# Optimization experiments

Hardware: AMD Instinct MI355X
Metric: run time of the kernel (lower is better)

## Reference

```python
import jax, jax.numpy as jnp
import numpy as np

LEVELS = 3


def _wavelet_pyramid(x, levels=LEVELS):
    """Faithful jax port of WaveletTransform.forward.

    Per level: take top-left (H/2^l, W/2^l) region, convolve with the 3x3
    separable low-pass kernel outer([.25,.5,.25]) using zero-padded 'same'
    conv (kernel is symmetric so scipy's flip is a no-op), then write the
    2x-strided downsample into the top-left quarter.
    """
    B, C, H, W = x.shape
    k1 = jnp.array([0.25, 0.5, 0.25], dtype=x.dtype)
    K = jnp.outer(k1, k1)[None, None]  # [1,1,3,3] low_pass.T @ low_pass
    result = x
    for level in range(levels):
        sh, sw = H // (2 ** level), W // (2 ** level)
        if min(sh, sw) <= 2:
            break
        # fold B,C into batch: per-channel 2D conv, zero boundary = scipy 'same'
        temp = result[:, :, :sh, :sw].reshape(B * C, 1, sh, sw)
        approx = jax.lax.conv_general_dilated(
            temp, K, window_strides=(1, 1), padding='SAME',
            dimension_numbers=('NCHW', 'OIHW', 'NCHW'))
        down = approx[:, :, ::2, ::2][:, :, :sh // 2, :sw // 2]
        result = result.at[:, :, :sh // 2, :sw // 2].set(
            down.reshape(B, C, sh // 2, sw // 2))
    return result


def setup_inputs() -> dict:
    key = jax.random.key(0)
    x = jax.random.normal(key, (8, 32, 512, 512), dtype=jnp.float32)
    return {"x": x}


def reference(x):
    return _wavelet_pyramid(x, LEVELS)
```

## Files before the change

### kernel.cpp

```cpp
#include <hip/hip_runtime.h>

#define W 512
#define IMG (512 * 512)
#define NIMG 256

__global__ __launch_bounds__(256) void kA(const float* __restrict__ x,
                                          float* __restrict__ out) {
    const int gid = blockIdx.x;
    const int img = gid >> 8;
    const int b   = gid & 255;
    const int tid = threadIdx.x;
    const int i = (b >> 2) * 4 + (tid >> 6);
    const int j = (b & 3) * 64 + (tid & 63);

    const float* xi = x + (size_t)img * IMG;
    float* oi = out + (size_t)img * IMG;

    const int r0 = 2 * i - 1, r1 = 2 * i, r2 = 2 * i + 1;
    const int c0 = 2 * j - 1;

    float2 m1 = *(const float2*)(xi + r1 * W + 2 * j);
    float2 m2 = *(const float2*)(xi + r2 * W + 2 * j);
    float2 m0 = (r0 >= 0) ? *(const float2*)(xi + r0 * W + 2 * j)
                          : make_float2(0.f, 0.f);
    float l0 = (r0 >= 0 && c0 >= 0) ? xi[r0 * W + c0] : 0.f;
    float l1 = (c0 >= 0) ? xi[r1 * W + c0] : 0.f;
    float l2 = (c0 >= 0) ? xi[r2 * W + c0] : 0.f;

    float h0 = 0.25f * l0 + 0.5f * m0.x + 0.25f * m0.y;
    float h1 = 0.25f * l1 + 0.5f * m1.x + 0.25f * m1.y;
    float h2 = 0.25f * l2 + 0.5f * m2.x + 0.25f * m2.y;
    oi[i * W + j] = 0.25f * h0 + 0.5f * h1 + 0.25f * h2;

    if (i >= 128 || j >= 128) {
        *(float2*)(oi + r1 * W + 2 * j) = m1;
        *(float2*)(oi + r2 * W + 2 * j) = m2;
    }
}

__global__ __launch_bounds__(1024) void kBC(float* __restrict__ out) {
    __shared__ float S1[128][128];
    const int img = blockIdx.x;
    float* oi = out + (size_t)img * IMG;
    const int tid = threadIdx.x;
    const int j = tid & 127;
    const int i0 = tid >> 7;

    for (int k = 0; k < 16; ++k) {
        const int i = i0 + 8 * k;
        const int r0 = 2 * i - 1, r1 = 2 * i, r2 = 2 * i + 1;
        const int c0 = 2 * j - 1;
        float2 m1 = *(const float2*)(oi + r1 * W + 2 * j);
        float2 m2 = *(const float2*)(oi + r2 * W + 2 * j);
        float2 m0 = (r0 >= 0) ? *(const float2*)(oi + r0 * W + 2 * j)
                              : make_float2(0.f, 0.f);
        float l0 = (r0 >= 0 && c0 >= 0) ? oi[r0 * W + c0] : 0.f;
        float l1 = (c0 >= 0) ? oi[r1 * W + c0] : 0.f;
        float l2 = (c0 >= 0) ? oi[r2 * W + c0] : 0.f;
        float h0 = 0.25f * l0 + 0.5f * m0.x + 0.25f * m0.y;
        float h1 = 0.25f * l1 + 0.5f * m1.x + 0.25f * m1.y;
        float h2 = 0.25f * l2 + 0.5f * m2.x + 0.25f * m2.y;
        S1[i][j] = 0.25f * h0 + 0.5f * h1 + 0.25f * h2;
    }
    __syncthreads();

    for (int k = 0; k < 16; ++k) {
        const int i = i0 + 8 * k;
        if (i >= 64 || j >= 64) oi[i * W + j] = S1[i][j];
    }

    const int j2 = tid & 63;
    const int ib = tid >> 6;
    for (int k = 0; k < 4; ++k) {
        const int i = ib + 16 * k;
        const int r0 = 2 * i - 1, r1 = 2 * i, r2 = 2 * i + 1;
        const int c0 = 2 * j2 - 1;
        float m1x = S1[r1][2 * j2], m1y = S1[r1][2 * j2 + 1];
        float m2x = S1[r2][2 * j2], m2y = S1[r2][2 * j2 + 1];
        float m0x = (r0 >= 0) ? S1[r0][2 * j2] : 0.f;
        float m0y = (r0 >= 0) ? S1[r0][2 * j2 + 1] : 0.f;
        float l0 = (r0 >= 0 && c0 >= 0) ? S1[r0][c0] : 0.f;
        float l1 = (c0 >= 0) ? S1[r1][c0] : 0.f;
        float l2 = (c0 >= 0) ? S1[r2][c0] : 0.f;
        float h0 = 0.25f * l0 + 0.5f * m0x + 0.25f * m0y;
        float h1 = 0.25f * l1 + 0.5f * m1x + 0.25f * m1y;
        float h2 = 0.25f * l2 + 0.5f * m2x + 0.25f * m2y;
        oi[i * W + j2] = 0.25f * h0 + 0.5f * h1 + 0.25f * h2;
    }
}

extern "C" void kernel_launch(void* const* d_in, const int* in_sizes, int n_in,
                              void* d_out, int out_size, void* d_ws,
                              size_t ws_size, hipStream_t stream) {
    const float* x = (const float*)d_in[0];
    float* out = (float*)d_out;
    (void)in_sizes; (void)n_in; (void)d_ws; (void)ws_size; (void)out_size;

    kA<<<NIMG * 256, 256, 0, stream>>>(x, out);
    kBC<<<NIMG, 1024, 0, stream>>>(out);
}
```

Before: 467.0 us.

## Vectorize loads with float4 plus wave shuffles and split level-2/3 into separate grids

```diff
diff --git a/kernel.cpp b/kernel.cpp
--- a/kernel.cpp
+++ b/kernel.cpp
@@ -3,89 +3,130 @@
 #define W 512
 #define IMG (512 * 512)
 #define NIMG 256
+#define L1SZ (128 * 128)
 
 __global__ __launch_bounds__(256) void kA(const float* __restrict__ x,
                                           float* __restrict__ out) {
     const int gid = blockIdx.x;
-    const int img = gid >> 8;
-    const int b   = gid & 255;
+    const int img = gid >> 7;
+    const int b   = gid & 127;
     const int tid = threadIdx.x;
-    const int i = (b >> 2) * 4 + (tid >> 6);
-    const int j = (b & 3) * 64 + (tid & 63);
+    const int lane = tid & 63;
+    const int i  = (b >> 1) * 4 + (tid >> 6);
+    const int jq = (b & 1) * 64 + lane;
+    const int c0 = 4 * jq;
 
     const float* xi = x + (size_t)img * IMG;
     float* oi = out + (size_t)img * IMG;
+    const int r0 = 2 * i - 1, r1 = 2 * i, r2 = 2 * i + 1;
 
-    const int r0 = 2 * i - 1, r1 = 2 * i, r2 = 2 * i + 1;
-    const int c0 = 2 * j - 1;
+    float4 m1 = *(const float4*)(xi + r1 * W + c0);
+    float4 m2 = *(const float4*)(xi + r2 * W + c0);
+    float4 m0 = (r0 >= 0) ? *(const float4*)(xi + r0 * W + c0)
+                          : make_float4(0.f, 0.f, 0.f, 0.f);
 
-    float2 m1 = *(const float2*)(xi + r1 * W + 2 * j);
-    float2 m2 = *(const float2*)(xi + r2 * W + 2 * j);
-    float2 m0 = (r0 >= 0) ? *(const float2*)(xi + r0 * W + 2 * j)
-                          : make_float2(0.f, 0.f);
-    float l0 = (r0 >= 0 && c0 >= 0) ? xi[r0 * W + c0] : 0.f;
-    float l1 = (c0 >= 0) ? xi[r1 * W + c0] : 0.f;
-    float l2 = (c0 >= 0) ? xi[r2 * W + c0] : 0.f;
+    float p0 = __shfl_up(m0.w, 1, 64);
+    float p1 = __shfl_up(m1.w, 1, 64);
+    float p2 = __shfl_up(m2.w, 1, 64);
+    if (lane == 0) {
+        if (c0 == 0) {
+            p0 = p1 = p2 = 0.f;
+        } else {
+            p1 = xi[r1 * W + c0 - 1];
+            p2 = xi[r2 * W + c0 - 1];
+            p0 = (r0 >= 0) ? xi[r0 * W + c0 - 1] : 0.f;
+        }
+    }
 
-    float h0 = 0.25f * l0 + 0.5f * m0.x + 0.25f * m0.y;
-    float h1 = 0.25f * l1 + 0.5f * m1.x + 0.25f * m1.y;
-    float h2 = 0.25f * l2 + 0.5f * m2.x + 0.25f * m2.y;
-    oi[i * W + j] = 0.25f * h0 + 0.5f * h1 + 0.25f * h2;
+    float ha0 = 0.25f * p0 + 0.5f * m0.x + 0.25f * m0.y;
+    float hb0 = 0.25f * m0.y + 0.5f * m0.z + 0.25f * m0.w;
+    float ha1 = 0.25f * p1 + 0.5f * m1.x + 0.25f * m1.y;
+    float hb1 = 0.25f * m1.y + 0.5f * m1.z + 0.25f * m1.w;
+    float ha2 = 0.25f * p2 + 0.5f * m2.x + 0.25f * m2.y;
+    float hb2 = 0.25f * m2.y + 0.5f * m2.z + 0.25f * m2.w;
+    float2 o;
+    o.x = 0.25f * ha0 + 0.5f * ha1 + 0.25f * ha2;
+    o.y = 0.25f * hb0 + 0.5f * hb1 + 0.25f * hb2;
+    *(float2*)(oi + i * W + 2 * jq) = o;
 
-    if (i >= 128 || j >= 128) {
-        *(float2*)(oi + r1 * W + 2 * j) = m1;
-        *(float2*)(oi + r2 * W + 2 * j) = m2;
+    if (i >= 128 || jq >= 64) {
+        *(float4*)(oi + r1 * W + c0) = m1;
+        *(float4*)(oi + r2 * W + c0) = m2;
     }
 }
 
-__global__ __launch_bounds__(1024) void kBC(float* __restrict__ out) {
-    __shared__ float S1[128][128];
-    const int img = blockIdx.x;
+__global__ __launch_bounds__(256) void kB(const float* __restrict__ out,
+                                          float* __restrict__ ws) {
+    const int gid = blockIdx.x;
+    const int img = gid >> 5;
+    const int b   = gid & 31;
+    const int tid = threadIdx.x;
+    const int lane = tid & 63;
+    const int i  = b * 4 + (tid >> 6);
+    const int c0 = 4 * lane;
+
+    const float* oi = out + (size_t)img * IMG;
+    float* wsi = ws + (size_t)img * L1SZ;
+    const int r0 = 2 * i - 1, r1 = 2 * i, r2 = 2 * i + 1;
+
+    float4 m1 = *(const float4*)(oi + r1 * W + c0);
+    float4 m2 = *(const float4*)(oi + r2 * W + c0);
+    float4 m0 = (r0 >= 0) ? *(const float4*)(oi + r0 * W + c0)
+                          : make_float4(0.f, 0.f, 0.f, 0.f);
+    float p0 = __shfl_up(m0.w, 1, 64);
+    float p1 = __shfl_up(m1.w, 1, 64);
+    float p2 = __shfl_up(m2.w, 1, 64);
+    if (lane == 0) { p0 = p1 = p2 = 0.f; }
+
+    float ha0 = 0.25f * p0 + 0.5f * m0.x + 0.25f * m0.y;
+    float hb0 = 0.25f * m0.y + 0.5f * m0.z + 0.25f * m0.w;
+    float ha1 = 0.25f * p1 + 0.5f * m1.x + 0.25f * m1.y;
+    float hb1 = 0.25f * m1.y + 0.5f * m1.z + 0.25f * m1.w;
+    float ha2 = 0.25f * p2 + 0.5f * m2.x + 0.25f * m2.y;
+    float hb2 = 0.25f * m2.y + 0.5f * m2.z + 0.25f * m2.w;
+    float2 o;
+    o.x = 0.25f * ha0 + 0.5f * ha1 + 0.25f * ha2;
+    o.y = 0.25f * hb0 + 0.5f * hb1 + 0.25f * hb2;
+    *(float2*)(wsi + i * 128 + 2 * lane) = o;
+}
+
+__global__ __launch_bounds__(256) void kC(const float* __restrict__ ws,
+                                          float* __restrict__ out) {
+    const int gid = blockIdx.x;
+    const int img = gid >> 3;
+    const int b   = gid & 7;
+    const int tid = threadIdx.x;
+    const int i2  = b * 8 + (tid >> 5);
+    const int jq2 = tid & 31;
+    const int c0  = 4 * jq2;
+
+    const float* wsi = ws + (size_t)img * L1SZ;
     float* oi = out + (size_t)img * IMG;
-    const int tid = threadIdx.x;
-    const int j = tid & 127;
-    const int i0 = tid >> 7;
+    const int r0 = 2 * i2 - 1, r1 = 2 * i2, r2 = 2 * i2 + 1;
 
-    for (int k = 0; k < 16; ++k) {
-        const int i = i0 + 8 * k;
-        const int r0 = 2 * i - 1, r1 = 2 * i, r2 = 2 * i + 1;
-        const int c0 = 2 * j - 1;
-        float2 m1 = *(const float2*)(oi + r1 * W + 2 * j);
-        float2 m2 = *(const float2*)(oi + r2 * W + 2 * j);
-        float2 m0 = (r0 >= 0) ? *(const float2*)(oi + r0 * W + 2 * j)
-                              : make_float2(0.f, 0.f);
-        float l0 = (r0 >= 0 && c0 >= 0) ? oi[r0 * W + c0] : 0.f;
-        float l1 = (c0 >= 0) ? oi[r1 * W + c0] : 0.f;
-        float l2 = (c0 >= 0) ? oi[r2 * W + c0] : 0.f;
-        float h0 = 0.25f * l0 + 0.5f * m0.x + 0.25f * m0.y;
-        float h1 = 0.25f * l1 + 0.5f * m1.x + 0.25f * m1.y;
-        float h2 = 0.25f * l2 + 0.5f * m2.x + 0.25f * m2.y;
-        S1[i][j] = 0.25f * h0 + 0.5f * h1 + 0.25f * h2;
-    }
-    __syncthreads();
+    float4 m1 = *(const float4*)(wsi + r1 * 128 + c0);
+    float4 m2 = *(const float4*)(wsi + r2 * 128 + c0);
+    float4 m0 = (r0 >= 0) ? *(const float4*)(wsi + r0 * 128 + c0)
+                          : make_float4(0.f, 0.f, 0.f, 0.f);
+    float p0 = __shfl_up(m0.w, 1, 64);
+    float p1 = __shfl_up(m1.w, 1, 64);
+    float p2 = __shfl_up(m2.w, 1, 64);
+    if (jq2 == 0) { p0 = p1 = p2 = 0.f; }
 
-    for (int k = 0; k < 16; ++k) {
-        const int i = i0 + 8 * k;
-        if (i >= 64 || j >= 64) oi[i * W + j] = S1[i][j];
-    }
+    float ha0 = 0.25f * p0 + 0.5f * m0.x + 0.25f * m0.y;
+    float hb0 = 0.25f * m0.y + 0.5f * m0.z + 0.25f * m0.w;
+    float ha1 = 0.25f * p1 + 0.5f * m1.x + 0.25f * m1.y;
+    float hb1 = 0.25f * m1.y + 0.5f * m1.z + 0.25f * m1.w;
+    float ha2 = 0.25f * p2 + 0.5f * m2.x + 0.25f * m2.y;
+    float hb2 = 0.25f * m2.y + 0.5f * m2.z + 0.25f * m2.w;
+    float2 o;
+    o.x = 0.25f * ha0 + 0.5f * ha1 + 0.25f * ha2;
+    o.y = 0.25f * hb0 + 0.5f * hb1 + 0.25f * hb2;
+    *(float2*)(oi + i2 * W + 2 * jq2) = o;
 
-    const int j2 = tid & 63;
-    const int ib = tid >> 6;
-    for (int k = 0; k < 4; ++k) {
-        const int i = ib + 16 * k;
-        const int r0 = 2 * i - 1, r1 = 2 * i, r2 = 2 * i + 1;
-        const int c0 = 2 * j2 - 1;
-        float m1x = S1[r1][2 * j2], m1y = S1[r1][2 * j2 + 1];
-        float m2x = S1[r2][2 * j2], m2y = S1[r2][2 * j2 + 1];
-        float m0x = (r0 >= 0) ? S1[r0][2 * j2] : 0.f;
-        float m0y = (r0 >= 0) ? S1[r0][2 * j2 + 1] : 0.f;
-        float l0 = (r0 >= 0 && c0 >= 0) ? S1[r0][c0] : 0.f;
-        float l1 = (c0 >= 0) ? S1[r1][c0] : 0.f;
-        float l2 = (c0 >= 0) ? S1[r2][c0] : 0.f;
-        float h0 = 0.25f * l0 + 0.5f * m0x + 0.25f * m0y;
-        float h1 = 0.25f * l1 + 0.5f * m1x + 0.25f * m1y;
-        float h2 = 0.25f * l2 + 0.5f * m2x + 0.25f * m2y;
-        oi[i * W + j2] = 0.25f * h0 + 0.5f * h1 + 0.25f * h2;
+    if (r1 >= 64 || c0 >= 64) {
+        *(float4*)(oi + r1 * W + c0) = m1;
+        *(float4*)(oi + r2 * W + c0) = m2;
     }
 }
 
@@ -94,8 +135,10 @@
                               size_t ws_size, hipStream_t stream) {
     const float* x = (const float*)d_in[0];
     float* out = (float*)d_out;
-    (void)in_sizes; (void)n_in; (void)d_ws; (void)ws_size; (void)out_size;
+    float* ws = (float*)d_ws;
+    (void)in_sizes; (void)n_in; (void)ws_size; (void)out_size;
 
-    kA<<<NIMG * 256, 256, 0, stream>>>(x, out);
-    kBC<<<NIMG, 1024, 0, stream>>>(out);
+    kA<<<NIMG * 128, 256, 0, stream>>>(x, out);
+    kB<<<NIMG * 32, 256, 0, stream>>>(out, ws);
+    kC<<<NIMG * 8, 256, 0, stream>>>(ws, out);
 }
```

Measured after the change: 457.7 us. 1.02x faster.
